# Kernel optimization log

Hardware: AMD Instinct MI355X
Metric: run time of the kernel (lower is better)

## Reference

```python
import jax, jax.numpy as jnp
import numpy as np

H = 16  # num heads

def setup_inputs() -> dict:
    key = jax.random.key(0)
    k1, k2, k3 = jax.random.split(key, 3)
    B, L, D = 2, 2048, 1024
    x = jax.random.normal(k1, (B, L, D), dtype=jnp.float32)
    # torch Linear weight is [out,in]; we store transposed [in,out] so y = x @ W
    w_qkv = jax.random.normal(k2, (D, 3 * D), dtype=jnp.float32) * (D ** -0.5)
    w_proj = jax.random.normal(k3, (D, D), dtype=jnp.float32) * (D ** -0.5)
    return {"x": x, "w_qkv": w_qkv, "w_proj": w_proj, "num_prefix_tokens": 256}

def _prefix_causal_mask(L: int, M: int):
    # True = masked. Strict upper triangle (causal), then text rows (M:) may
    # see ALL prefix columns (:M).
    mask = jnp.triu(jnp.ones((L, L), dtype=bool), k=1)
    mask = mask.at[M:, :M].set(False)
    return mask

def reference(x, w_qkv, w_proj, num_prefix_tokens):
    B, L, D = x.shape
    d = D // H
    scale = d ** -0.5
    qkv = (x @ w_qkv).reshape(B, L, 3, H, d)
    q = jnp.transpose(qkv[:, :, 0], (0, 2, 1, 3))  # [B,H,L,d]
    k = jnp.transpose(qkv[:, :, 1], (0, 2, 1, 3))
    v = jnp.transpose(qkv[:, :, 2], (0, 2, 1, 3))
    logits = jnp.einsum("bhqd,bhkd->bhqk", q, k) * scale  # [B,H,L,L]
    mask = _prefix_causal_mask(L, num_prefix_tokens)
    logits = jnp.where(mask[None, None], -jnp.inf, logits)
    attn = jax.nn.softmax(logits, axis=-1)
    out = jnp.einsum("bhqk,bhkd->bhqd", attn, v)  # [B,H,L,d]
    out = jnp.transpose(out, (0, 2, 1, 3)).reshape(B, L, D)
    return out @ w_proj
```

## Files before the change

### kernel.cpp

```cpp
#include <hip/hip_runtime.h>
#include <hip/hip_bf16.h>

#define BATCH   2
#define L_SEQ   2048
#define DMODEL  1024
#define NHEADS  16
#define DHEAD   64
#define SEG     (BATCH*NHEADS*L_SEQ*DHEAD)

typedef __attribute__((ext_vector_type(8)))  short bf16x8;
typedef __attribute__((ext_vector_type(4)))  float f32x4;
typedef __attribute__((ext_vector_type(16))) float f32x16;

__device__ __forceinline__ unsigned short f2b(float f) {
    unsigned int u = __float_as_uint(f);
    return (unsigned short)((u + 0x7FFFu + ((u >> 16) & 1u)) >> 16);
}
__device__ __forceinline__ unsigned int pk2(float a, float b) {
    __hip_bfloat162 h = __float22bfloat162_rn(make_float2(a, b));
    return *(unsigned int*)&h;
}
__device__ __forceinline__ void glds16(const unsigned short* g, unsigned short* l) {
    __builtin_amdgcn_global_load_lds(
        (const __attribute__((address_space(1))) unsigned int*)g,
        (__attribute__((address_space(3))) unsigned int*)l, 16, 0, 0);
}

__device__ __forceinline__ void tcast64(const float* __restrict__ in,
                                        unsigned short* __restrict__ out,
                                        int K, int N, int bx, int by, int t) {
    __shared__ unsigned short T[64][65];
    const int k0 = by * 64, n0 = bx * 64;
    const int r = t >> 4, c4 = (t & 15) * 4;
#pragma unroll
    for (int rep = 0; rep < 4; ++rep) {
        int kk = rep * 16 + r;
        float4 f = *(const float4*)&in[(size_t)(k0 + kk) * N + n0 + c4];
        T[kk][c4 + 0] = f2b(f.x);
        T[kk][c4 + 1] = f2b(f.y);
        T[kk][c4 + 2] = f2b(f.z);
        T[kk][c4 + 3] = f2b(f.w);
    }
    __syncthreads();
#pragma unroll
    for (int rep = 0; rep < 4; ++rep) {
        int nn = rep * 16 + r;
        ushort4 o;
        o.x = T[c4 + 0][nn];
        o.y = T[c4 + 1][nn];
        o.z = T[c4 + 2][nn];
        o.w = T[c4 + 3][nn];
        *(ushort4*)&out[(size_t)(n0 + nn) * K + k0 + c4] = o;
    }
}

__global__ __launch_bounds__(256)
void prep(const float* __restrict__ x, const float* __restrict__ wqkv,
          const float* __restrict__ wproj, unsigned short* __restrict__ xb,
          unsigned short* __restrict__ wqkvT, unsigned short* __restrict__ wprojT) {
    const int id = blockIdx.x, t = threadIdx.x;
    if (id < 4096) {
        int i = id * 1024 + t * 4;
        float4 f = *(const float4*)&x[i];
        ushort4 o;
        o.x = f2b(f.x); o.y = f2b(f.y); o.z = f2b(f.z); o.w = f2b(f.w);
        *(ushort4*)&xb[i] = o;
    } else if (id < 4864) {
        int lid = id - 4096;
        tcast64(wqkv, wqkvT, DMODEL, 3 * DMODEL, lid % 48, lid / 48, t);
    } else {
        int lid = id - 4864;
        tcast64(wproj, wprojT, DMODEL, DMODEL, lid & 15, lid >> 4, t);
    }
}

__global__ __launch_bounds__(256)
void gemm_qkv(const unsigned short* __restrict__ A, const unsigned short* __restrict__ Bt,
              unsigned short* __restrict__ Cb) {
    __shared__ unsigned short SLDS[128 * 128];
    unsigned short* Asm = SLDS;
    unsigned short* Bsm = SLDS + 128 * 64;

    const int t = threadIdx.x;
    const int lane = t & 63, wave = t >> 6;
    const int quad = lane >> 4, l16 = lane & 15;
    const int wm = (wave >> 1) * 64, wn = (wave & 1) * 64;
    const int id = blockIdx.y * gridDim.x + blockIdx.x;
    const int xcd = id & 7, sq = id >> 3;
    const int m0 = (xcd * 4 + sq / 24) * 128;
    const int n0 = (sq % 24) * 128;
    const bool vrole = (n0 >= 2048);

    const int gsw = (lane & 7) ^ (lane >> 3);
    const unsigned short* ga[4];
    const unsigned short* gb[4];
    unsigned short* la[4];
    unsigned short* lb[4];
#pragma unroll
    for (int i = 0; i < 4; ++i) {
        int row = wave * 32 + i * 8 + (lane >> 3);
        ga[i] = &A[(size_t)(m0 + row) * DMODEL + gsw * 8];
        gb[i] = &Bt[(size_t)(n0 + row) * DMODEL + gsw * 8];
        la[i] = &Asm[(wave * 32 + i * 8) * 64];
        lb[i] = &Bsm[(wave * 32 + i * 8) * 64];
    }
    const int sx = l16 & 7;

    f32x4 acc[4][4];
#pragma unroll
    for (int i = 0; i < 4; ++i)
#pragma unroll
        for (int j = 0; j < 4; ++j)
#pragma unroll
            for (int r = 0; r < 4; ++r) acc[i][j][r] = 0.0f;

    for (int k0 = 0; k0 < DMODEL; k0 += 64) {
        __syncthreads();
#pragma unroll
        for (int i = 0; i < 4; ++i) {
            glds16(ga[i] + k0, la[i]);
            glds16(gb[i] + k0, lb[i]);
        }
        __syncthreads();
#pragma unroll
        for (int s = 0; s < 2; ++s) {
            bf16x8 af[4], bfr[4];
#pragma unroll
            for (int i = 0; i < 4; ++i)
                af[i] = *(const bf16x8*)&Asm[(wm + i * 16 + l16) * 64 + ((4 * s + quad) ^ sx) * 8];
#pragma unroll
            for (int j = 0; j < 4; ++j)
                bfr[j] = *(const bf16x8*)&Bsm[(wn + j * 16 + l16) * 64 + ((4 * s + quad) ^ sx) * 8];
            if (!vrole) {
#pragma unroll
                for (int i = 0; i < 4; ++i)
#pragma unroll
                    for (int j = 0; j < 4; ++j)
                        acc[i][j] = __builtin_amdgcn_mfma_f32_16x16x32_bf16(af[i], bfr[j], acc[i][j], 0, 0, 0);
            } else {
#pragma unroll
                for (int i = 0; i < 4; ++i)
#pragma unroll
                    for (int j = 0; j < 4; ++j)
                        acc[i][j] = __builtin_amdgcn_mfma_f32_16x16x32_bf16(bfr[j], af[i], acc[i][j], 0, 0, 0);
            }
        }
    }

    const float qscale = 0.1803368801111244f;
    const float scl = (!vrole && n0 < 1024) ? qscale : 1.0f;
    __syncthreads();
#pragma unroll
    for (int i = 0; i < 4; ++i)
#pragma unroll
        for (int r = 0; r < 4; ++r) {
#pragma unroll
            for (int j = 0; j < 4; ++j) {
                int row_l, col_l;
                if (!vrole) {
                    row_l = wm + i * 16 + quad * 4 + r;
                    col_l = wn + j * 16 + l16;
                } else {
                    row_l = wn + j * 16 + quad * 4 + r;
                    col_l = wm + i * 16 + l16;
                }
                int key = row_l & 7;
                SLDS[row_l * 128 + (((col_l >> 3) ^ key) * 8) + (col_l & 7)] =
                    f2b(acc[i][j][r] * scl);
            }
        }
    __syncthreads();

    const int s0 = n0 >> 10;
    const int bb = m0 >> 11;
#pragma unroll
    for (int it = 0; it < 4; ++it) {
        int row = it * 32 + (t >> 3);
        int c = t & 7;
        int key = row & 7;
        bf16x8 v0 = *(const bf16x8*)&SLDS[row * 128 + ((c ^ key) * 8)];
        bf16x8 v1 = *(const bf16x8*)&SLDS[row * 128 + (((c + 8) ^ key) * 8)];
        if (!vrole) {
            int token = m0 + row, lp = token & (L_SEQ - 1);
            int n_a = n0 + c * 8,        h_a = (n_a >> 6) & 15, d_a = n_a & 63;
            int n_b = n0 + (c + 8) * 8,  h_b = (n_b >> 6) & 15, d_b = n_b & 63;
            size_t base = (size_t)s0 * SEG;
            *(bf16x8*)&Cb[base + (((size_t)(bb * NHEADS + h_a) * L_SEQ + lp) * DHEAD) + d_a] = v0;
            *(bf16x8*)&Cb[base + (((size_t)(bb * NHEADS + h_b) * L_SEQ + lp) * DHEAD) + d_b] = v1;
        } else {
            int fr = (n0 - 2048) + row;
            int h = fr >> 6, dd = fr & 63;
            int lp0 = (m0 & (L_SEQ - 1));
            size_t base = 2 * (size_t)SEG +
                          (((size_t)(bb * NHEADS + h) * DHEAD + dd) * L_SEQ) + lp0;
            *(bf16x8*)&Cb[base + c * 8]       = v0;
            *(bf16x8*)&Cb[base + (c + 8) * 8] = v1;
        }
    }
}

__global__ __launch_bounds__(256)
void gemm_proj(const unsigned short* __restrict__ A, const unsigned short* __restrict__ Bt,
               float* __restrict__ Cf) {
    __shared__ unsigned short Asm[64 * 64];
    __shared__ unsigned short Bsm[64 * 64];

    const int t = threadIdx.x;
    const int lane = t & 63, wave = t >> 6;
    const int quad = lane >> 4, l16 = lane & 15;
    const int wm = (wave >> 1) * 32, wn = (wave & 1) * 32;
    const int id = blockIdx.y * gridDim.x + blockIdx.x;
    const int xcd = id & 7, sq = id >> 3;
    const int m0 = (xcd * 8 + (sq >> 4)) * 64;
    const int n0 = (sq & 15) * 64;
    const int K = DMODEL, N = DMODEL;

    const int gsw = (lane & 7) ^ (lane >> 3);
    const unsigned short* ga[2];
    const unsigned short* gb[2];
    unsigned short* la[2];
    unsigned short* lb[2];
#pragma unroll
    for (int i = 0; i < 2; ++i) {
        int row = wave * 8 + i * 32 + (lane >> 3);
        ga[i] = &A[(size_t)(m0 + row) * K + gsw * 8];
        gb[i] = &Bt[(size_t)(n0 + row) * K + gsw * 8];
        la[i] = &Asm[(wave * 8 + i * 32) * 64];
        lb[i] = &Bsm[(wave * 8 + i * 32) * 64];
    }
    const int sx = l16 & 7;

    f32x4 acc[2][2];
#pragma unroll
    for (int i = 0; i < 2; ++i)
#pragma unroll
        for (int j = 0; j < 2; ++j)
#pragma unroll
            for (int r = 0; r < 4; ++r) acc[i][j][r] = 0.0f;

    for (int k0 = 0; k0 < K; k0 += 64) {
        __syncthreads();
#pragma unroll
        for (int i = 0; i < 2; ++i) {
            glds16(ga[i] + k0, la[i]);
            glds16(gb[i] + k0, lb[i]);
        }
        __syncthreads();
#pragma unroll
        for (int s = 0; s < 2; ++s) {
            bf16x8 af[2], bfr[2];
#pragma unroll
            for (int i = 0; i < 2; ++i)
                af[i] = *(const bf16x8*)&Asm[(wm + i * 16 + l16) * 64 + ((4 * s + quad) ^ sx) * 8];
#pragma unroll
            for (int j = 0; j < 2; ++j)
                bfr[j] = *(const bf16x8*)&Bsm[(wn + j * 16 + l16) * 64 + ((4 * s + quad) ^ sx) * 8];
#pragma unroll
            for (int i = 0; i < 2; ++i)
#pragma unroll
                for (int j = 0; j < 2; ++j)
                    acc[i][j] = __builtin_amdgcn_mfma_f32_16x16x32_bf16(af[i], bfr[j], acc[i][j], 0, 0, 0);
        }
    }

#pragma unroll
    for (int i = 0; i < 2; ++i)
#pragma unroll
        for (int r = 0; r < 4; ++r) {
            int row = m0 + wm + i * 16 + quad * 4 + r;
#pragma unroll
            for (int j = 0; j < 2; ++j)
                Cf[(size_t)row * N + n0 + wn + j * 16 + l16] = acc[i][j][r];
        }
}

__global__ __launch_bounds__(256)
void attn_mfma(const unsigned short* __restrict__ Qg, const unsigned short* __restrict__ Kg,
               const unsigned short* __restrict__ Vg, unsigned short* __restrict__ Ao) {
    __shared__ unsigned short Ksm[128 * 64];
    __shared__ unsigned short Vsm[64 * 128];
    __shared__ unsigned short Psm[4 * 32 * 64];

    const int t = threadIdx.x;
    const int lane = t & 63, wave = t >> 6;
    const int l31 = lane & 31, hi = lane >> 5;
    const int bh = blockIdx.x & 31;
    const int Qt = 31 - (blockIdx.x >> 5);
    const int q0 = Qt * 64;
    const int qh = wave & 1, kp = wave >> 1;
    const int wq0 = q0 + qh * 32;
    const int nstrip = (Qt >> 1) + 1;
    const int b = bh >> 4, h = bh & 15;
    const size_t qkbase = (size_t)bh * L_SEQ * DHEAD;
    const size_t vbase  = (size_t)bh * DHEAD * L_SEQ;

    bf16x8 bq[4];
#pragma unroll
    for (int ks = 0; ks < 4; ++ks)
        bq[ks] = *(const bf16x8*)&Qg[qkbase + (size_t)(wq0 + l31) * DHEAD + ks * 16 + hi * 8];

    const int kc0 = t & 7,  kr0 = (t >> 3) * 4;
    const int vc0 = t & 15, vd0 = (t >> 4) * 4;

    unsigned short* Pw = Psm + wave * 32 * 64;

    f32x16 O0, O1;
#pragma unroll
    for (int r = 0; r < 16; ++r) { O0[r] = 0.0f; O1[r] = 0.0f; }
    float rs = 0.0f;

    bf16x8 gk[4], gv[4];
#pragma unroll
    for (int i = 0; i < 4; ++i) {
        gk[i] = *(const bf16x8*)&Kg[qkbase + (size_t)(kr0 + i) * DHEAD + kc0 * 8];
        gv[i] = *(const bf16x8*)&Vg[vbase + (size_t)(vd0 + i) * L_SEQ + vc0 * 8];
    }

    for (int s = 0; s < nstrip; ++s) {
        __syncthreads();
#pragma unroll
        for (int i = 0; i < 4; ++i) {
            *(bf16x8*)&Ksm[(kc0 * 128 + ((kr0 + i) ^ kc0)) * 8] = gk[i];
            *(bf16x8*)&Vsm[(vc0 * 64 + ((vd0 + i) ^ vc0)) * 8] = gv[i];
        }
        if (s + 1 < nstrip) {
            const int kn = (s + 1) * 128;
#pragma unroll
            for (int i = 0; i < 4; ++i) {
                gk[i] = *(const bf16x8*)&Kg[qkbase + (size_t)(kn + kr0 + i) * DHEAD + kc0 * 8];
                gv[i] = *(const bf16x8*)&Vg[vbase + (size_t)(vd0 + i) * L_SEQ + kn + vc0 * 8];
            }
        }
        __syncthreads();

        const int keybase = s * 128 + kp * 64;
        if (keybase <= wq0 + 31) {
            f32x16 ST[2];
#pragma unroll
            for (int kh = 0; kh < 2; ++kh) {
#pragma unroll
                for (int r = 0; r < 16; ++r) ST[kh][r] = 0.0f;
#pragma unroll
                for (int ks = 0; ks < 4; ++ks) {
                    const int c = ks * 2 + hi;
                    const int rk = kp * 64 + kh * 32 + l31;
                    bf16x8 a = *(const bf16x8*)&Ksm[(c * 128 + (rk ^ c)) * 8];
                    ST[kh] = __builtin_amdgcn_mfma_f32_32x32x16_bf16(a, bq[ks], ST[kh], 0, 0, 0);
                }
            }

            if (keybase + 63 > wq0) {
                const int qg = wq0 + l31;
#pragma unroll
                for (int kh = 0; kh < 2; ++kh)
#pragma unroll
                    for (int r = 0; r < 16; ++r) {
                        int keyg = keybase + kh * 32 + (r & 3) + 8 * (r >> 2) + 4 * hi;
                        if (keyg > qg) ST[kh][r] = -1e30f;
                    }
            }

#pragma unroll
            for (int kh = 0; kh < 2; ++kh)
#pragma unroll
                for (int g = 0; g < 4; ++g) {
                    float p0 = __builtin_amdgcn_exp2f(ST[kh][4 * g + 0]);
                    float p1 = __builtin_amdgcn_exp2f(ST[kh][4 * g + 1]);
                    float p2 = __builtin_amdgcn_exp2f(ST[kh][4 * g + 2]);
                    float p3 = __builtin_amdgcn_exp2f(ST[kh][4 * g + 3]);
                    rs += (p0 + p1) + (p2 + p3);
                    const int c = kh * 4 + g;
                    *(uint2*)&Pw[(c * 32 + (l31 ^ c)) * 8 + hi * 4] =
                        make_uint2(pk2(p0, p1), pk2(p2, p3));
                }

#pragma unroll
            for (int ks = 0; ks < 4; ++ks) {
                const int cp = ks * 2 + hi;
                const int cv = kp * 8 + ks * 2 + hi;
                bf16x8 pa = *(const bf16x8*)&Pw[(cp * 32 + (l31 ^ cp)) * 8];
                bf16x8 v0 = *(const bf16x8*)&Vsm[(cv * 64 + (l31 ^ cv)) * 8];
                bf16x8 v1 = *(const bf16x8*)&Vsm[(cv * 64 + ((32 + l31) ^ cv)) * 8];
                O0 = __builtin_amdgcn_mfma_f32_32x32x16_bf16(pa, v0, O0, 0, 0, 0);
                O1 = __builtin_amdgcn_mfma_f32_32x32x16_bf16(pa, v1, O1, 0, 0, 0);
            }
        }
    }

    rs += __shfl_xor(rs, 32, 64);

    __syncthreads();
    float* Oex = (float*)Ksm;
    float* Rex = (float*)Vsm;
    if (kp == 1) {
#pragma unroll
        for (int r = 0; r < 16; ++r) {
            int qloc = (r & 3) + 8 * (r >> 2) + 4 * hi;
            Oex[qh * 2048 + qloc * 64 + l31]      = O0[r];
            Oex[qh * 2048 + qloc * 64 + 32 + l31] = O1[r];
        }
        if (hi == 0) Rex[qh * 32 + l31] = rs;
    }
    __syncthreads();
    if (kp == 0) {
        float rs_tot = rs + Rex[qh * 32 + l31];
        float linv = 1.0f / rs_tot;
        float lf[16];
#pragma unroll
        for (int r = 0; r < 16; ++r) {
            int qloc = (r & 3) + 8 * (r >> 2) + 4 * hi;
            O0[r] += Oex[qh * 2048 + qloc * 64 + l31];
            O1[r] += Oex[qh * 2048 + qloc * 64 + 32 + l31];
            lf[r] = __shfl(linv, qloc, 32);
        }
#pragma unroll
        for (int r = 0; r < 16; ++r) {
            int qloc = (r & 3) + 8 * (r >> 2) + 4 * hi;
            int token = wq0 + qloc;
            size_t ob = ((size_t)(b * L_SEQ + token)) * DMODEL + h * DHEAD;
            Ao[ob + l31]      = f2b(O0[r] * lf[r]);
            Ao[ob + 32 + l31] = f2b(O1[r] * lf[r]);
        }
    }
}

extern "C" void kernel_launch(void* const* d_in, const int* in_sizes, int n_in,
                              void* d_out, int out_size, void* d_ws, size_t ws_size,
                              hipStream_t stream) {
    const float* x      = (const float*)d_in[0];
    const float* w_qkv  = (const float*)d_in[1];
    const float* w_proj = (const float*)d_in[2];
    float* out = (float*)d_out;

    unsigned short* ws     = (unsigned short*)d_ws;
    unsigned short* xb     = ws;
    unsigned short* wqkvT  = xb + 4194304;
    unsigned short* wprojT = wqkvT + 3145728;
    unsigned short* qkv    = wprojT + 1048576;
    unsigned short* ao     = qkv + 3 * (size_t)SEG;

    prep<<<5120, 256, 0, stream>>>(x, w_qkv, w_proj, xb, wqkvT, wprojT);

    gemm_qkv<<<dim3(24, 32), 256, 0, stream>>>(xb, wqkvT, qkv);

    attn_mfma<<<1024, 256, 0, stream>>>(qkv, qkv + SEG, qkv + 2 * (size_t)SEG, ao);

    gemm_proj<<<dim3(16, 64), 256, 0, stream>>>(ao, wprojT, out);
}
```

Baseline: 178.5 us.

## Rewrite QKV and projection GEMMs with larger tiles and 4-stage async LDS pipeline

Both GEMMs move to 512-thread blocks with larger output tiles (256x256 for QKV, 128x128 for proj) and a 4-slot ring buffer of K=32 slices. Loads for three stages ahead are issued with global_load_lds while the current slice runs through MFMAs, using explicit vmcnt waits and raw barriers in place of a full sync every step. The MFMA sections, including those in attention, are wrapped in s_setprio. The aim is to hide global-memory latency and raise data reuse per tile, at the cost of more LDS (128KB for QKV), higher register pressure and fewer blocks, which could hurt occupancy and wave-level balance.

```diff
diff --git a/kernel.cpp b/kernel.cpp
--- a/kernel.cpp
+++ b/kernel.cpp
@@ -25,6 +25,11 @@
         (const __attribute__((address_space(1))) unsigned int*)g,
         (__attribute__((address_space(3))) unsigned int*)l, 16, 0, 0);
 }
+
+#define SBAR()  __builtin_amdgcn_s_barrier()
+#define LGKM0() do { asm volatile("s_waitcnt lgkmcnt(0)" ::: "memory"); \
+                     __builtin_amdgcn_sched_barrier(0); } while (0)
+#define VMCNT(n) asm volatile("s_waitcnt vmcnt(" #n ")" ::: "memory")
 
 __device__ __forceinline__ void tcast64(const float* __restrict__ in,
                                         unsigned short* __restrict__ out,
@@ -74,203 +79,236 @@
     }
 }
 
-__global__ __launch_bounds__(256)
+__global__ __launch_bounds__(512, 2)
 void gemm_qkv(const unsigned short* __restrict__ A, const unsigned short* __restrict__ Bt,
               unsigned short* __restrict__ Cb) {
-    __shared__ unsigned short SLDS[128 * 128];
-    unsigned short* Asm = SLDS;
-    unsigned short* Bsm = SLDS + 128 * 64;
+    __shared__ unsigned short SLDS[65536];
 
     const int t = threadIdx.x;
     const int lane = t & 63, wave = t >> 6;
     const int quad = lane >> 4, l16 = lane & 15;
-    const int wm = (wave >> 1) * 64, wn = (wave & 1) * 64;
-    const int id = blockIdx.y * gridDim.x + blockIdx.x;
+    const int wm = (wave >> 2) * 128, wn = (wave & 3) * 64;
+
+    const int id = blockIdx.x;
     const int xcd = id & 7, sq = id >> 3;
-    const int m0 = (xcd * 4 + sq / 24) * 128;
-    const int n0 = (sq % 24) * 128;
+    const int m0 = (xcd * 2 + sq / 12) * 256;
+    const int n0 = (sq % 12) * 256;
     const bool vrole = (n0 >= 2048);
 
-    const int gsw = (lane & 7) ^ (lane >> 3);
-    const unsigned short* ga[4];
-    const unsigned short* gb[4];
-    unsigned short* la[4];
-    unsigned short* lb[4];
-#pragma unroll
-    for (int i = 0; i < 4; ++i) {
-        int row = wave * 32 + i * 8 + (lane >> 3);
-        ga[i] = &A[(size_t)(m0 + row) * DMODEL + gsw * 8];
-        gb[i] = &Bt[(size_t)(n0 + row) * DMODEL + gsw * 8];
-        la[i] = &Asm[(wave * 32 + i * 8) * 64];
-        lb[i] = &Bsm[(wave * 32 + i * 8) * 64];
-    }
-    const int sx = l16 & 7;
-
-    f32x4 acc[4][4];
-#pragma unroll
-    for (int i = 0; i < 4; ++i)
+    const int srow = lane >> 2;
+    const int gch  = (lane & 3) ^ ((srow >> 1) & 3);
+    const unsigned short* gA[2];
+    const unsigned short* gB[2];
+    int ldA[2], ldB[2];
+#pragma unroll
+    for (int j = 0; j < 2; ++j) {
+        int r = j * 128 + wave * 16 + srow;
+        gA[j] = &A [(size_t)(m0 + r) * DMODEL + gch * 8];
+        gB[j] = &Bt[(size_t)(n0 + r) * DMODEL + gch * 8];
+        ldA[j] = (j * 128 + wave * 16) * 32;
+        ldB[j] = 8192 + (j * 128 + wave * 16) * 32;
+    }
+
+    f32x4 acc[8][4];
+#pragma unroll
+    for (int i = 0; i < 8; ++i)
 #pragma unroll
         for (int j = 0; j < 4; ++j)
 #pragma unroll
             for (int r = 0; r < 4; ++r) acc[i][j][r] = 0.0f;
 
-    for (int k0 = 0; k0 < DMODEL; k0 += 64) {
-        __syncthreads();
-#pragma unroll
-        for (int i = 0; i < 4; ++i) {
-            glds16(ga[i] + k0, la[i]);
-            glds16(gb[i] + k0, lb[i]);
-        }
-        __syncthreads();
-#pragma unroll
-        for (int s = 0; s < 2; ++s) {
-            bf16x8 af[4], bfr[4];
+#pragma unroll
+    for (int s = 0; s < 3; ++s) {
+        const int so = s * 16384, ko = s * 32;
+#pragma unroll
+        for (int j = 0; j < 2; ++j) {
+            glds16(gA[j] + ko, &SLDS[so + ldA[j]]);
+            glds16(gB[j] + ko, &SLDS[so + ldB[j]]);
+        }
+    }
+    __syncthreads();
+
+    const int key = (l16 >> 1) & 3;
+#pragma unroll 4
+    for (int S = 0; S < 32; ++S) {
+        const int slot  = (S & 3) * 16384;
+        const int wslot = ((S + 3) & 3) * 16384;
+        const int ko    = (S + 3 < 32 ? S + 3 : 31) * 32;
+        bf16x8 af[4], bf[4];
+
+#pragma unroll
+        for (int i = 0; i < 4; ++i)
+            af[i] = *(const bf16x8*)&SLDS[slot + (wm + i * 16 + l16) * 32 + ((quad ^ key) * 8)];
+#pragma unroll
+        for (int j = 0; j < 4; ++j)
+            bf[j] = *(const bf16x8*)&SLDS[slot + 8192 + (wn + j * 16 + l16) * 32 + ((quad ^ key) * 8)];
+        glds16(gA[0] + ko, &SLDS[wslot + ldA[0]]);
+        glds16(gA[1] + ko, &SLDS[wslot + ldA[1]]);
+        SBAR();
+        LGKM0();
+        __builtin_amdgcn_s_setprio(1);
+        if (!vrole) {
 #pragma unroll
             for (int i = 0; i < 4; ++i)
-                af[i] = *(const bf16x8*)&Asm[(wm + i * 16 + l16) * 64 + ((4 * s + quad) ^ sx) * 8];
-#pragma unroll
-            for (int j = 0; j < 4; ++j)
-                bfr[j] = *(const bf16x8*)&Bsm[(wn + j * 16 + l16) * 64 + ((4 * s + quad) ^ sx) * 8];
-            if (!vrole) {
-#pragma unroll
-                for (int i = 0; i < 4; ++i)
-#pragma unroll
-                    for (int j = 0; j < 4; ++j)
-                        acc[i][j] = __builtin_amdgcn_mfma_f32_16x16x32_bf16(af[i], bfr[j], acc[i][j], 0, 0, 0);
-            } else {
-#pragma unroll
-                for (int i = 0; i < 4; ++i)
-#pragma unroll
-                    for (int j = 0; j < 4; ++j)
-                        acc[i][j] = __builtin_amdgcn_mfma_f32_16x16x32_bf16(bfr[j], af[i], acc[i][j], 0, 0, 0);
-            }
-        }
-    }
-
+#pragma unroll
+                for (int j = 0; j < 4; ++j)
+                    acc[i][j] = __builtin_amdgcn_mfma_f32_16x16x32_bf16(af[i], bf[j], acc[i][j], 0, 0, 0);
+        } else {
+#pragma unroll
+            for (int i = 0; i < 4; ++i)
+#pragma unroll
+                for (int j = 0; j < 4; ++j)
+                    acc[i][j] = __builtin_amdgcn_mfma_f32_16x16x32_bf16(bf[j], af[i], acc[i][j], 0, 0, 0);
+        }
+        __builtin_amdgcn_s_setprio(0);
+        SBAR();
+
+#pragma unroll
+        for (int i = 0; i < 4; ++i)
+            af[i] = *(const bf16x8*)&SLDS[slot + (wm + 64 + i * 16 + l16) * 32 + ((quad ^ key) * 8)];
+        glds16(gB[0] + ko, &SLDS[wslot + ldB[0]]);
+        glds16(gB[1] + ko, &SLDS[wslot + ldB[1]]);
+        SBAR();
+        LGKM0();
+        __builtin_amdgcn_s_setprio(1);
+        if (!vrole) {
+#pragma unroll
+            for (int i = 0; i < 4; ++i)
+#pragma unroll
+                for (int j = 0; j < 4; ++j)
+                    acc[4 + i][j] = __builtin_amdgcn_mfma_f32_16x16x32_bf16(af[i], bf[j], acc[4 + i][j], 0, 0, 0);
+        } else {
+#pragma unroll
+            for (int i = 0; i < 4; ++i)
+#pragma unroll
+                for (int j = 0; j < 4; ++j)
+                    acc[4 + i][j] = __builtin_amdgcn_mfma_f32_16x16x32_bf16(bf[j], af[i], acc[4 + i][j], 0, 0, 0);
+        }
+        __builtin_amdgcn_s_setprio(0);
+        VMCNT(8);
+        SBAR();
+    }
+
+    VMCNT(0);
+    SBAR();
     const float qscale = 0.1803368801111244f;
     const float scl = (!vrole && n0 < 1024) ? qscale : 1.0f;
-    __syncthreads();
-#pragma unroll
-    for (int i = 0; i < 4; ++i)
-#pragma unroll
-        for (int r = 0; r < 4; ++r) {
-#pragma unroll
-            for (int j = 0; j < 4; ++j) {
-                int row_l, col_l;
-                if (!vrole) {
-                    row_l = wm + i * 16 + quad * 4 + r;
-                    col_l = wn + j * 16 + l16;
-                } else {
-                    row_l = wn + j * 16 + quad * 4 + r;
-                    col_l = wm + i * 16 + l16;
+#pragma unroll
+    for (int mh = 0; mh < 2; ++mh)
+#pragma unroll
+        for (int i = 0; i < 4; ++i)
+#pragma unroll
+            for (int j = 0; j < 4; ++j)
+#pragma unroll
+                for (int r = 0; r < 4; ++r) {
+                    int row_l, col_l;
+                    if (!vrole) {
+                        row_l = wm + mh * 64 + i * 16 + quad * 4 + r;
+                        col_l = wn + j * 16 + l16;
+                    } else {
+                        row_l = wn + j * 16 + quad * 4 + r;
+                        col_l = wm + mh * 64 + i * 16 + l16;
+                    }
+                    SLDS[row_l * 256 + (((col_l >> 3) ^ (row_l & 7)) * 8) + (col_l & 7)] =
+                        f2b(acc[mh * 4 + i][j][r] * scl);
                 }
-                int key = row_l & 7;
-                SLDS[row_l * 128 + (((col_l >> 3) ^ key) * 8) + (col_l & 7)] =
-                    f2b(acc[i][j][r] * scl);
-            }
-        }
-    __syncthreads();
-
-    const int s0 = n0 >> 10;
+    __syncthreads();
+
     const int bb = m0 >> 11;
 #pragma unroll
-    for (int it = 0; it < 4; ++it) {
-        int row = it * 32 + (t >> 3);
-        int c = t & 7;
-        int key = row & 7;
-        bf16x8 v0 = *(const bf16x8*)&SLDS[row * 128 + ((c ^ key) * 8)];
-        bf16x8 v1 = *(const bf16x8*)&SLDS[row * 128 + (((c + 8) ^ key) * 8)];
+    for (int it = 0; it < 16; ++it) {
+        int row = it * 16 + (t >> 5);
+        int c = t & 31;
+        bf16x8 v = *(const bf16x8*)&SLDS[row * 256 + ((c ^ (row & 7)) * 8)];
         if (!vrole) {
             int token = m0 + row, lp = token & (L_SEQ - 1);
-            int n_a = n0 + c * 8,        h_a = (n_a >> 6) & 15, d_a = n_a & 63;
-            int n_b = n0 + (c + 8) * 8,  h_b = (n_b >> 6) & 15, d_b = n_b & 63;
-            size_t base = (size_t)s0 * SEG;
-            *(bf16x8*)&Cb[base + (((size_t)(bb * NHEADS + h_a) * L_SEQ + lp) * DHEAD) + d_a] = v0;
-            *(bf16x8*)&Cb[base + (((size_t)(bb * NHEADS + h_b) * L_SEQ + lp) * DHEAD) + d_b] = v1;
+            int n = n0 + c * 8;
+            int h = (n >> 6) & 15, d = n & 63, s0 = n >> 10;
+            *(bf16x8*)&Cb[(size_t)s0 * SEG +
+                          (((size_t)(bb * NHEADS + h) * L_SEQ + lp) * DHEAD) + d] = v;
         } else {
             int fr = (n0 - 2048) + row;
             int h = fr >> 6, dd = fr & 63;
-            int lp0 = (m0 & (L_SEQ - 1));
-            size_t base = 2 * (size_t)SEG +
-                          (((size_t)(bb * NHEADS + h) * DHEAD + dd) * L_SEQ) + lp0;
-            *(bf16x8*)&Cb[base + c * 8]       = v0;
-            *(bf16x8*)&Cb[base + (c + 8) * 8] = v1;
-        }
-    }
-}
-
-__global__ __launch_bounds__(256)
+            *(bf16x8*)&Cb[2 * (size_t)SEG +
+                          (((size_t)(bb * NHEADS + h) * DHEAD + dd) * L_SEQ) +
+                          (m0 & (L_SEQ - 1)) + c * 8] = v;
+        }
+    }
+}
+
+__global__ __launch_bounds__(512, 2)
 void gemm_proj(const unsigned short* __restrict__ A, const unsigned short* __restrict__ Bt,
                float* __restrict__ Cf) {
-    __shared__ unsigned short Asm[64 * 64];
-    __shared__ unsigned short Bsm[64 * 64];
+    __shared__ unsigned short SLDS[32768];
 
     const int t = threadIdx.x;
     const int lane = t & 63, wave = t >> 6;
     const int quad = lane >> 4, l16 = lane & 15;
-    const int wm = (wave >> 1) * 32, wn = (wave & 1) * 32;
-    const int id = blockIdx.y * gridDim.x + blockIdx.x;
+    const int wm = (wave >> 2) * 64, wn = (wave & 3) * 32;
+
+    const int id = blockIdx.x;
     const int xcd = id & 7, sq = id >> 3;
-    const int m0 = (xcd * 8 + (sq >> 4)) * 64;
-    const int n0 = (sq & 15) * 64;
-    const int K = DMODEL, N = DMODEL;
-
-    const int gsw = (lane & 7) ^ (lane >> 3);
-    const unsigned short* ga[2];
-    const unsigned short* gb[2];
-    unsigned short* la[2];
-    unsigned short* lb[2];
-#pragma unroll
-    for (int i = 0; i < 2; ++i) {
-        int row = wave * 8 + i * 32 + (lane >> 3);
-        ga[i] = &A[(size_t)(m0 + row) * K + gsw * 8];
-        gb[i] = &Bt[(size_t)(n0 + row) * K + gsw * 8];
-        la[i] = &Asm[(wave * 8 + i * 32) * 64];
-        lb[i] = &Bsm[(wave * 8 + i * 32) * 64];
-    }
-    const int sx = l16 & 7;
-
-    f32x4 acc[2][2];
-#pragma unroll
-    for (int i = 0; i < 2; ++i)
+    const int m0 = (xcd * 4 + (sq >> 3)) * 128;
+    const int n0 = (sq & 7) * 128;
+
+    const int srow = lane >> 2;
+    const int gch  = (lane & 3) ^ ((srow >> 1) & 3);
+    const unsigned short* gA = &A [(size_t)(m0 + wave * 16 + srow) * DMODEL + gch * 8];
+    const unsigned short* gB = &Bt[(size_t)(n0 + wave * 16 + srow) * DMODEL + gch * 8];
+    const int ldA = (wave * 16) * 32;
+    const int ldB = 4096 + (wave * 16) * 32;
+
+    f32x4 acc[4][2];
+#pragma unroll
+    for (int i = 0; i < 4; ++i)
 #pragma unroll
         for (int j = 0; j < 2; ++j)
 #pragma unroll
             for (int r = 0; r < 4; ++r) acc[i][j][r] = 0.0f;
 
-    for (int k0 = 0; k0 < K; k0 += 64) {
-        __syncthreads();
-#pragma unroll
-        for (int i = 0; i < 2; ++i) {
-            glds16(ga[i] + k0, la[i]);
-            glds16(gb[i] + k0, lb[i]);
-        }
-        __syncthreads();
-#pragma unroll
-        for (int s = 0; s < 2; ++s) {
-            bf16x8 af[2], bfr[2];
-#pragma unroll
-            for (int i = 0; i < 2; ++i)
-                af[i] = *(const bf16x8*)&Asm[(wm + i * 16 + l16) * 64 + ((4 * s + quad) ^ sx) * 8];
+#pragma unroll
+    for (int s = 0; s < 3; ++s) {
+        glds16(gA + s * 32, &SLDS[s * 8192 + ldA]);
+        glds16(gB + s * 32, &SLDS[s * 8192 + ldB]);
+    }
+    __syncthreads();
+
+    const int key = (l16 >> 1) & 3;
+#pragma unroll 4
+    for (int S = 0; S < 32; ++S) {
+        const int slot  = (S & 3) * 8192;
+        const int wslot = ((S + 3) & 3) * 8192;
+        const int ko    = (S + 3 < 32 ? S + 3 : 31) * 32;
+        bf16x8 af[4], bf[2];
+#pragma unroll
+        for (int i = 0; i < 4; ++i)
+            af[i] = *(const bf16x8*)&SLDS[slot + (wm + i * 16 + l16) * 32 + ((quad ^ key) * 8)];
+#pragma unroll
+        for (int j = 0; j < 2; ++j)
+            bf[j] = *(const bf16x8*)&SLDS[slot + 4096 + (wn + j * 16 + l16) * 32 + ((quad ^ key) * 8)];
+        glds16(gA + ko, &SLDS[wslot + ldA]);
+        glds16(gB + ko, &SLDS[wslot + ldB]);
+        SBAR();
+        LGKM0();
+        __builtin_amdgcn_s_setprio(1);
+#pragma unroll
+        for (int i = 0; i < 4; ++i)
 #pragma unroll
             for (int j = 0; j < 2; ++j)
-                bfr[j] = *(const bf16x8*)&Bsm[(wn + j * 16 + l16) * 64 + ((4 * s + quad) ^ sx) * 8];
-#pragma unroll
-            for (int i = 0; i < 2; ++i)
-#pragma unroll
-                for (int j = 0; j < 2; ++j)
-                    acc[i][j] = __builtin_amdgcn_mfma_f32_16x16x32_bf16(af[i], bfr[j], acc[i][j], 0, 0, 0);
-        }
-    }
-
-#pragma unroll
-    for (int i = 0; i < 2; ++i)
+                acc[i][j] = __builtin_amdgcn_mfma_f32_16x16x32_bf16(af[i], bf[j], acc[i][j], 0, 0, 0);
+        __builtin_amdgcn_s_setprio(0);
+        VMCNT(4);
+        SBAR();
+    }
+
+#pragma unroll
+    for (int i = 0; i < 4; ++i)
 #pragma unroll
         for (int r = 0; r < 4; ++r) {
             int row = m0 + wm + i * 16 + quad * 4 + r;
 #pragma unroll
             for (int j = 0; j < 2; ++j)
-                Cf[(size_t)row * N + n0 + wn + j * 16 + l16] = acc[i][j][r];
+                Cf[(size_t)row * DMODEL + n0 + wn + j * 16 + l16] = acc[i][j][r];
         }
 }
 
@@ -336,6 +374,7 @@
         const int keybase = s * 128 + kp * 64;
         if (keybase <= wq0 + 31) {
             f32x16 ST[2];
+            __builtin_amdgcn_s_setprio(1);
 #pragma unroll
             for (int kh = 0; kh < 2; ++kh) {
 #pragma unroll
@@ -348,6 +387,7 @@
                     ST[kh] = __builtin_amdgcn_mfma_f32_32x32x16_bf16(a, bq[ks], ST[kh], 0, 0, 0);
                 }
             }
+            __builtin_amdgcn_s_setprio(0);
 
             if (keybase + 63 > wq0) {
                 const int qg = wq0 + l31;
@@ -374,6 +414,7 @@
                         make_uint2(pk2(p0, p1), pk2(p2, p3));
                 }
 
+            __builtin_amdgcn_s_setprio(1);
 #pragma unroll
             for (int ks = 0; ks < 4; ++ks) {
                 const int cp = ks * 2 + hi;
@@ -384,6 +425,7 @@
                 O0 = __builtin_amdgcn_mfma_f32_32x32x16_bf16(pa, v0, O0, 0, 0, 0);
                 O1 = __builtin_amdgcn_mfma_f32_32x32x16_bf16(pa, v1, O1, 0, 0, 0);
             }
+            __builtin_amdgcn_s_setprio(0);
         }
     }
 
@@ -441,9 +483,9 @@
 
     prep<<<5120, 256, 0, stream>>>(x, w_qkv, w_proj, xb, wqkvT, wprojT);
 
-    gemm_qkv<<<dim3(24, 32), 256, 0, stream>>>(xb, wqkvT, qkv);
+    gemm_qkv<<<192, 512, 0, stream>>>(xb, wqkvT, qkv);
 
     attn_mfma<<<1024, 256, 0, stream>>>(qkv, qkv + SEG, qkv + 2 * (size_t)SEG, ao);
 
-    gemm_proj<<<dim3(16, 64), 256, 0, stream>>>(ao, wprojT, out);
-}
+    gemm_proj<<<256, 512, 0, stream>>>(ao, wprojT, out);
+}
```

After: 212.9 us. 19.2% more time.

## Double-buffer LDS in GEMMs, enlarge proj tiles, add MFMA priority hints

Applied to the files above, without the earlier changes.

Both GEMM kernels now keep two LDS buffers, so the global-to-LDS load of the next K tile is issued before the MFMAs on the current tile, and each iteration needs one barrier instead of two. The projection GEMM moves from 64x64 to 128x128 tiles, giving more reuse per load, with its grid cut to 256 blocks. s_setprio raises wave priority around the MFMA sections in the GEMMs and in attention. The cost is double the LDS per block (64 KB), which lowers occupancy, and the proj grid is now smaller than the CU count.

```diff
diff --git a/kernel.cpp b/kernel.cpp
--- a/kernel.cpp
+++ b/kernel.cpp
@@ -77,9 +77,7 @@
 __global__ __launch_bounds__(256)
 void gemm_qkv(const unsigned short* __restrict__ A, const unsigned short* __restrict__ Bt,
               unsigned short* __restrict__ Cb) {
-    __shared__ unsigned short SLDS[128 * 128];
-    unsigned short* Asm = SLDS;
-    unsigned short* Bsm = SLDS + 128 * 64;
+    __shared__ unsigned short SLDS[2 * 128 * 128];
 
     const int t = threadIdx.x;
     const int lane = t & 63, wave = t >> 6;
@@ -94,15 +92,14 @@
     const int gsw = (lane & 7) ^ (lane >> 3);
     const unsigned short* ga[4];
     const unsigned short* gb[4];
-    unsigned short* la[4];
-    unsigned short* lb[4];
+    int ldA[4], ldB[4];
 #pragma unroll
     for (int i = 0; i < 4; ++i) {
         int row = wave * 32 + i * 8 + (lane >> 3);
         ga[i] = &A[(size_t)(m0 + row) * DMODEL + gsw * 8];
         gb[i] = &Bt[(size_t)(n0 + row) * DMODEL + gsw * 8];
-        la[i] = &Asm[(wave * 32 + i * 8) * 64];
-        lb[i] = &Bsm[(wave * 32 + i * 8) * 64];
+        ldA[i] = (wave * 32 + i * 8) * 64;
+        ldB[i] = 8192 + (wave * 32 + i * 8) * 64;
     }
     const int sx = l16 & 7;
 
@@ -114,14 +111,26 @@
 #pragma unroll
             for (int r = 0; r < 4; ++r) acc[i][j][r] = 0.0f;
 
-    for (int k0 = 0; k0 < DMODEL; k0 += 64) {
-        __syncthreads();
-#pragma unroll
-        for (int i = 0; i < 4; ++i) {
-            glds16(ga[i] + k0, la[i]);
-            glds16(gb[i] + k0, lb[i]);
-        }
-        __syncthreads();
+#pragma unroll
+    for (int i = 0; i < 4; ++i) {
+        glds16(ga[i], &SLDS[ldA[i]]);
+        glds16(gb[i], &SLDS[ldB[i]]);
+    }
+    __syncthreads();
+
+    int cur = 0;
+    for (int kt = 0; kt < 16; ++kt) {
+        if (kt < 15) {
+            const int ko = (kt + 1) * 64;
+            unsigned short* dst = &SLDS[(cur ^ 1) * 16384];
+#pragma unroll
+            for (int i = 0; i < 4; ++i) {
+                glds16(ga[i] + ko, dst + ldA[i]);
+                glds16(gb[i] + ko, dst + ldB[i]);
+            }
+        }
+        const unsigned short* Asm = &SLDS[cur * 16384];
+        const unsigned short* Bsm = Asm + 8192;
 #pragma unroll
         for (int s = 0; s < 2; ++s) {
             bf16x8 af[4], bfr[4];
@@ -131,6 +140,7 @@
 #pragma unroll
             for (int j = 0; j < 4; ++j)
                 bfr[j] = *(const bf16x8*)&Bsm[(wn + j * 16 + l16) * 64 + ((4 * s + quad) ^ sx) * 8];
+            __builtin_amdgcn_s_setprio(1);
             if (!vrole) {
 #pragma unroll
                 for (int i = 0; i < 4; ++i)
@@ -144,12 +154,14 @@
                     for (int j = 0; j < 4; ++j)
                         acc[i][j] = __builtin_amdgcn_mfma_f32_16x16x32_bf16(bfr[j], af[i], acc[i][j], 0, 0, 0);
             }
-        }
+            __builtin_amdgcn_s_setprio(0);
+        }
+        __syncthreads();
+        cur ^= 1;
     }
 
     const float qscale = 0.1803368801111244f;
     const float scl = (!vrole && n0 < 1024) ? qscale : 1.0f;
-    __syncthreads();
 #pragma unroll
     for (int i = 0; i < 4; ++i)
 #pragma unroll
@@ -202,75 +214,88 @@
 __global__ __launch_bounds__(256)
 void gemm_proj(const unsigned short* __restrict__ A, const unsigned short* __restrict__ Bt,
                float* __restrict__ Cf) {
-    __shared__ unsigned short Asm[64 * 64];
-    __shared__ unsigned short Bsm[64 * 64];
+    __shared__ unsigned short SLDS[2 * 128 * 128];
 
     const int t = threadIdx.x;
     const int lane = t & 63, wave = t >> 6;
     const int quad = lane >> 4, l16 = lane & 15;
-    const int wm = (wave >> 1) * 32, wn = (wave & 1) * 32;
+    const int wm = (wave >> 1) * 64, wn = (wave & 1) * 64;
     const int id = blockIdx.y * gridDim.x + blockIdx.x;
     const int xcd = id & 7, sq = id >> 3;
-    const int m0 = (xcd * 8 + (sq >> 4)) * 64;
-    const int n0 = (sq & 15) * 64;
-    const int K = DMODEL, N = DMODEL;
+    const int m0 = (xcd * 4 + (sq >> 3)) * 128;
+    const int n0 = (sq & 7) * 128;
 
     const int gsw = (lane & 7) ^ (lane >> 3);
-    const unsigned short* ga[2];
-    const unsigned short* gb[2];
-    unsigned short* la[2];
-    unsigned short* lb[2];
-#pragma unroll
-    for (int i = 0; i < 2; ++i) {
-        int row = wave * 8 + i * 32 + (lane >> 3);
-        ga[i] = &A[(size_t)(m0 + row) * K + gsw * 8];
-        gb[i] = &Bt[(size_t)(n0 + row) * K + gsw * 8];
-        la[i] = &Asm[(wave * 8 + i * 32) * 64];
-        lb[i] = &Bsm[(wave * 8 + i * 32) * 64];
+    const unsigned short* ga[4];
+    const unsigned short* gb[4];
+    int ldA[4], ldB[4];
+#pragma unroll
+    for (int i = 0; i < 4; ++i) {
+        int row = wave * 32 + i * 8 + (lane >> 3);
+        ga[i] = &A[(size_t)(m0 + row) * DMODEL + gsw * 8];
+        gb[i] = &Bt[(size_t)(n0 + row) * DMODEL + gsw * 8];
+        ldA[i] = (wave * 32 + i * 8) * 64;
+        ldB[i] = 8192 + (wave * 32 + i * 8) * 64;
     }
     const int sx = l16 & 7;
 
-    f32x4 acc[2][2];
-#pragma unroll
-    for (int i = 0; i < 2; ++i)
-#pragma unroll
-        for (int j = 0; j < 2; ++j)
+    f32x4 acc[4][4];
+#pragma unroll
+    for (int i = 0; i < 4; ++i)
+#pragma unroll
+        for (int j = 0; j < 4; ++j)
 #pragma unroll
             for (int r = 0; r < 4; ++r) acc[i][j][r] = 0.0f;
 
-    for (int k0 = 0; k0 < K; k0 += 64) {
+#pragma unroll
+    for (int i = 0; i < 4; ++i) {
+        glds16(ga[i], &SLDS[ldA[i]]);
+        glds16(gb[i], &SLDS[ldB[i]]);
+    }
+    __syncthreads();
+
+    int cur = 0;
+    for (int kt = 0; kt < 16; ++kt) {
+        if (kt < 15) {
+            const int ko = (kt + 1) * 64;
+            unsigned short* dst = &SLDS[(cur ^ 1) * 16384];
+#pragma unroll
+            for (int i = 0; i < 4; ++i) {
+                glds16(ga[i] + ko, dst + ldA[i]);
+                glds16(gb[i] + ko, dst + ldB[i]);
+            }
+        }
+        const unsigned short* Asm = &SLDS[cur * 16384];
+        const unsigned short* Bsm = Asm + 8192;
+#pragma unroll
+        for (int s = 0; s < 2; ++s) {
+            bf16x8 af[4], bfr[4];
+#pragma unroll
+            for (int i = 0; i < 4; ++i)
+                af[i] = *(const bf16x8*)&Asm[(wm + i * 16 + l16) * 64 + ((4 * s + quad) ^ sx) * 8];
+#pragma unroll
+            for (int j = 0; j < 4; ++j)
+                bfr[j] = *(const bf16x8*)&Bsm[(wn + j * 16 + l16) * 64 + ((4 * s + quad) ^ sx) * 8];
+            __builtin_amdgcn_s_setprio(1);
+#pragma unroll
+            for (int i = 0; i < 4; ++i)
+#pragma unroll
+                for (int j = 0; j < 4; ++j)
+                    acc[i][j] = __builtin_amdgcn_mfma_f32_16x16x32_bf16(af[i], bfr[j], acc[i][j], 0, 0, 0);
+            __builtin_amdgcn_s_setprio(0);
+        }
         __syncthreads();
-#pragma unroll
-        for (int i = 0; i < 2; ++i) {
-            glds16(ga[i] + k0, la[i]);
-            glds16(gb[i] + k0, lb[i]);
-        }
-        __syncthreads();
-#pragma unroll
-        for (int s = 0; s < 2; ++s) {
-            bf16x8 af[2], bfr[2];
-#pragma unroll
-            for (int i = 0; i < 2; ++i)
-                af[i] = *(const bf16x8*)&Asm[(wm + i * 16 + l16) * 64 + ((4 * s + quad) ^ sx) * 8];
-#pragma unroll
-            for (int j = 0; j < 2; ++j)
-                bfr[j] = *(const bf16x8*)&Bsm[(wn + j * 16 + l16) * 64 + ((4 * s + quad) ^ sx) * 8];
-#pragma unroll
-            for (int i = 0; i < 2; ++i)
-#pragma unroll
-                for (int j = 0; j < 2; ++j)
-                    acc[i][j] = __builtin_amdgcn_mfma_f32_16x16x32_bf16(af[i], bfr[j], acc[i][j], 0, 0, 0);
-        }
-    }
-
-#pragma unroll
-    for (int i = 0; i < 2; ++i)
+        cur ^= 1;
+    }
+
+#pragma unroll
+    for (int i = 0; i < 4; ++i)
 #pragma unroll
         for (int r = 0; r < 4; ++r) {
             int row = m0 + wm + i * 16 + quad * 4 + r;
 #pragma unroll
-            for (int j = 0; j < 2; ++j)
-                Cf[(size_t)row * N + n0 + wn + j * 16 + l16] = acc[i][j][r];
+            for (int j = 0; j < 4; ++j)
+                Cf[(size_t)row * DMODEL + n0 + wn + j * 16 + l16] = acc[i][j][r];
         }
 }
 
@@ -336,6 +361,7 @@
         const int keybase = s * 128 + kp * 64;
         if (keybase <= wq0 + 31) {
             f32x16 ST[2];
+            __builtin_amdgcn_s_setprio(1);
 #pragma unroll
             for (int kh = 0; kh < 2; ++kh) {
 #pragma unroll
@@ -348,6 +374,7 @@
                     ST[kh] = __builtin_amdgcn_mfma_f32_32x32x16_bf16(a, bq[ks], ST[kh], 0, 0, 0);
                 }
             }
+            __builtin_amdgcn_s_setprio(0);
 
             if (keybase + 63 > wq0) {
                 const int qg = wq0 + l31;
@@ -374,6 +401,7 @@
                         make_uint2(pk2(p0, p1), pk2(p2, p3));
                 }
 
+            __builtin_amdgcn_s_setprio(1);
 #pragma unroll
             for (int ks = 0; ks < 4; ++ks) {
                 const int cp = ks * 2 + hi;
@@ -384,6 +412,7 @@
                 O0 = __builtin_amdgcn_mfma_f32_32x32x16_bf16(pa, v0, O0, 0, 0, 0);
                 O1 = __builtin_amdgcn_mfma_f32_32x32x16_bf16(pa, v1, O1, 0, 0, 0);
             }
+            __builtin_amdgcn_s_setprio(0);
         }
     }
 
@@ -445,5 +474,5 @@
 
     attn_mfma<<<1024, 256, 0, stream>>>(qkv, qkv + SEG, qkv + 2 * (size_t)SEG, ao);
 
-    gemm_proj<<<dim3(16, 64), 256, 0, stream>>>(ao, wprojT, out);
-}
+    gemm_proj<<<dim3(8, 32), 256, 0, stream>>>(ao, wprojT, out);
+}
```

Measured after the change: 176.6 us. Within noise of the previous version (-1.1%).
